# Optimization experiments

Measured on AMD Instinct MI355X. Metric: run time of the kernel, lower is better.

Reference implementation:

```python
import jax, jax.numpy as jnp
import numpy as np

B, L, C, H, W = 2, 4, 64, 80, 80
DISCRETE_RATIO, DOWNSAMPLE_RATE, NUM_ITER = 0.4, 2, 2


def _conv2d(x, w, b):
    y = jax.lax.conv_general_dilated(x, w, (1, 1), 'SAME',
                                     dimension_numbers=('NCHW', 'OIHW', 'NCHW'))
    return y + b[None, :, None, None]


def _get_transformation_matrix(M, h, w):
    # shift(center) @ [R 0; 0 1] @ shift(-center), then add raw translation (kornia-style)
    R = M[:, :2, :2]
    center = jnp.array([w / 2.0, h / 2.0], M.dtype)
    trans = center[None, :] - jnp.einsum('nij,j->ni', R, center) + M[:, :, 2]
    return jnp.concatenate([R, trans[:, :, None]], axis=2)  # (N,2,3)


def _warp_affine(src, M, mode):
    # src (N,C,h,w); M (N,2,3) maps src pixels -> dst pixels; sample src at M^{-1} @ dst
    # (equivalent to F.affine_grid/grid_sample with align_corners=True, zeros padding)
    N, Cc, h, w = src.shape
    bottom = jnp.tile(jnp.array([[[0.0, 0.0, 1.0]]], src.dtype), (N, 1, 1))
    Minv = jnp.linalg.inv(jnp.concatenate([M, bottom], axis=1))
    yy, xx = jnp.meshgrid(jnp.arange(h, dtype=src.dtype),
                          jnp.arange(w, dtype=src.dtype), indexing='ij')
    pts = jnp.stack([xx.ravel(), yy.ravel(), jnp.ones(h * w, src.dtype)], 0)  # (3,P)
    sp = jnp.einsum('nij,jp->nip', Minv, pts)
    sx, sy = sp[:, 0], sp[:, 1]  # (N,P) source pixel coords
    flat = src.reshape(N, Cc, h * w)

    def gather(ix, iy):
        valid = ((ix >= 0) & (ix < w) & (iy >= 0) & (iy < h)).astype(src.dtype)
        idx = jnp.clip(iy, 0, h - 1) * w + jnp.clip(ix, 0, w - 1)
        vals = jnp.take_along_axis(flat, jnp.broadcast_to(idx[:, None, :], (N, Cc, h * w)), axis=2)
        return vals * valid[:, None, :]

    if mode == 'nearest':
        out = gather(jnp.round(sx).astype(jnp.int32), jnp.round(sy).astype(jnp.int32))
    else:
        x0 = jnp.floor(sx); y0 = jnp.floor(sy)
        fx = (sx - x0)[:, None, :]; fy = (sy - y0)[:, None, :]
        x0 = x0.astype(jnp.int32); y0 = y0.astype(jnp.int32)
        out = (gather(x0, y0) * (1 - fx) * (1 - fy)
               + gather(x0 + 1, y0) * fx * (1 - fy)
               + gather(x0, y0 + 1) * (1 - fx) * fy
               + gather(x0 + 1, y0 + 1) * fx * fy)
    return out.reshape(N, Cc, h, w)


def _forward(x, pairwise_t_matrix, msg_w, msg_b, gates_w, gates_b, can_w, can_b, mlp_w, mlp_b):
    feats = x.reshape(B, L, C, H, W)
    # rows [0,1], cols [0,1,3] of the 4x4 SE(3) matrices; discretize translation
    t = pairwise_t_matrix[..., :2, :][..., jnp.array([0, 1, 3])]  # (B,L,L,2,3)
    t = t.at[..., 2].set(t[..., 2] / (DISCRETE_RATIO * DOWNSAMPLE_RATE))
    T = _get_transformation_matrix(t.reshape(-1, 2, 3), H, W)  # (B*L*L,2,3), flat index (b, j, i)
    mask = _warp_affine(jnp.ones((B * L * L, 1, H, W), x.dtype), T, 'nearest').reshape(B, L, L, 1, H, W)

    for _ in range(NUM_ITER):
        # 'b c h w -> b c w h' + flip(last): coordinate-convention fix (H==W)
        y = jnp.flip(jnp.swapaxes(feats, -1, -2), axis=-1)  # (B,L,C,H,W)
        # warp neighbor j into ego i frame with T[b,j,i]
        src = jnp.broadcast_to(y[:, :, None], (B, L, L, C, H, W)).reshape(-1, C, H, W)
        neighbor = _warp_affine(src, T, 'bilinear')
        ego = jnp.broadcast_to(y[:, None], (B, L, L, C, H, W)).reshape(-1, C, H, W)
        msg = _conv2d(jnp.concatenate([neighbor, ego], axis=1), msg_w, msg_b)
        msg = msg.reshape(B, L, L, C, H, W) * mask
        agg = msg.mean(axis=1)  # 'avg' over neighbors j -> (B,L,C,H,W)
        cat_feat = jnp.concatenate([y, agg], axis=2).reshape(B * L, 2 * C, H, W)
        # single ConvGRU step with zero initial hidden state
        h0 = jnp.zeros((B * L, C, H, W), x.dtype)
        gates = _conv2d(jnp.concatenate([cat_feat, h0], axis=1), gates_w, gates_b)
        reset = jax.nn.sigmoid(gates[:, :C])
        update = jax.nn.sigmoid(gates[:, C:])
        cand = jnp.tanh(_conv2d(jnp.concatenate([cat_feat, reset * h0], axis=1), can_w, can_b))
        h1 = (1.0 - update) * h0 + update * cand
        # undo the coordinate fix: flip(last) then 'c w h -> c h w'
        feats = jnp.swapaxes(jnp.flip(h1.reshape(B, L, C, H, W), axis=-1), -1, -2)

    out = feats[:, 0]  # ego agent of each sample, (B,C,H,W)
    return jnp.einsum('bchw,oc->bhwo', out, mlp_w) + mlp_b  # nn.Linear on channel-last


def setup_inputs() -> dict:
    key = jax.random.key(0)
    ks = jax.random.split(key, 12)
    x = jax.random.normal(ks[0], (B * L, C, H, W), dtype=jnp.float32)
    record_len = jnp.full((B,), L, dtype=jnp.int32)
    # realistic SE(2) pairwise transforms embedded in 4x4 homogeneous matrices
    ang = jax.random.uniform(ks[1], (B, L, L), minval=-0.3, maxval=0.3)
    tx = jax.random.uniform(ks[2], (B, L, L), minval=-8.0, maxval=8.0)
    ty = jax.random.uniform(ks[3], (B, L, L), minval=-8.0, maxval=8.0)
    c, s = jnp.cos(ang), jnp.sin(ang)
    z, o = jnp.zeros_like(ang), jnp.ones_like(ang)
    pairwise_t_matrix = jnp.stack([c, -s, z, tx,
                                   s, c, z, ty,
                                   z, z, o, z,
                                   z, z, z, o], axis=-1).reshape(B, L, L, 4, 4).astype(jnp.float32)
    prior_encoding = jax.random.normal(ks[4], (B * L, 3), dtype=jnp.float32)  # unused by forward
    sc = 0.05
    return {
        'x': x,
        'record_len': record_len,
        'pairwise_t_matrix': pairwise_t_matrix,
        'prior_encoding': prior_encoding,
        'msg_w': jax.random.normal(ks[5], (C, 2 * C, 3, 3), dtype=jnp.float32) * sc,
        'msg_b': jnp.zeros((C,), jnp.float32),
        'gates_w': jax.random.normal(ks[6], (2 * C, 3 * C, 3, 3), dtype=jnp.float32) * sc,
        'gates_b': jnp.zeros((2 * C,), jnp.float32),
        'can_w': jax.random.normal(ks[7], (C, 3 * C, 3, 3), dtype=jnp.float32) * sc,
        'can_b': jnp.zeros((C,), jnp.float32),
        'mlp_w': jax.random.normal(ks[8], (C, C), dtype=jnp.float32) * sc,
        'mlp_b': jnp.zeros((C,), jnp.float32),
    }


def reference(x, record_len, pairwise_t_matrix, prior_encoding,
              msg_w, msg_b, gates_w, gates_b, can_w, can_b, mlp_w, mlp_b):
    # record_len is fixed to L for every sample; prior_encoding is unused by the torch forward
    return _forward(x, pairwise_t_matrix, msg_w, msg_b, gates_w, gates_b,
                    can_w, can_b, mlp_w, mlp_b)
```

## Files before the change

kernel.cpp:

```cpp
#include <hip/hip_runtime.h>
#include <math.h>

#define WD 80
#define HW 6400
#define PW 82
#define PPX 6790
#define NIMG 8
#define NPAIR 32
#define TSTG 960

typedef short bf16x8 __attribute__((ext_vector_type(8)));
typedef float f32x4 __attribute__((ext_vector_type(4)));

__device__ __forceinline__ float bf2f(unsigned short u) {
    return __uint_as_float(((unsigned)u) << 16);
}
__device__ __forceinline__ unsigned short f2bf(float f) {
    unsigned u = __float_as_uint(f);
    u += 0x7fff + ((u >> 16) & 1);
    return (unsigned short)(u >> 16);
}

__device__ __forceinline__ void inv_affine(const float* __restrict__ P, int p, float* a) {
    const float* m = P + p * 16;
    float m00 = m[0], m01 = m[1], m02 = m[3] / 0.8f;
    float m10 = m[4], m11 = m[5], m12 = m[7] / 0.8f;
    float cx = 40.0f, cy = 40.0f;
    float tx = cx - (m00 * cx + m01 * cy) + m02;
    float ty = cy - (m10 * cx + m11 * cy) + m12;
    float id = 1.0f / (m00 * m11 - m01 * m10);
    a[0] =  m11 * id; a[1] = -m01 * id;
    a[3] = -m10 * id; a[4] =  m00 * id;
    a[2] = -(a[0] * tx + a[1] * ty);
    a[5] = -(a[3] * tx + a[4] * ty);
}

__global__ void prologue(const float* __restrict__ P, float* __restrict__ mats,
                         float* __restrict__ mask,
                         const float* __restrict__ msg_w, const float* __restrict__ gates_w,
                         const float* __restrict__ can_w,
                         unsigned short* __restrict__ Wn, unsigned short* __restrict__ We,
                         unsigned short* __restrict__ Wu, unsigned short* __restrict__ Wc) {
    int bx = blockIdx.x;
    if (bx < 32) {
        int p = bx;
        float a[6];
        inv_affine(P, p, a);
        if (threadIdx.x < 6) mats[p * 6 + threadIdx.x] = a[threadIdx.x];
        for (int q = threadIdx.x; q < HW; q += blockDim.x) {
            float x = (float)(q % WD), y = (float)(q / WD);
            float sx = a[0] * x + a[1] * y + a[2];
            float sy = a[3] * x + a[4] * y + a[5];
            int ix = (int)rintf(sx), iy = (int)rintf(sy);
            mask[p * HW + q] = (ix >= 0 && ix < WD && iy >= 0 && iy < WD) ? 1.0f : 0.0f;
        }
        return;
    }
    int t = (bx - 32) * 256 + threadIdx.x;
    if (t >= 221184) return;
    const float* src; unsigned short* dst;
    int cin_n, co_off, ci_off, stride, u;
    if (t < 36864)       { src = msg_w;   dst = Wn; cin_n = 64;  co_off = 0;  ci_off = 0;  stride = 1152; u = t; }
    else if (t < 73728)  { src = msg_w;   dst = We; cin_n = 64;  co_off = 0;  ci_off = 64; stride = 1152; u = t - 36864; }
    else if (t < 147456) { src = gates_w; dst = Wu; cin_n = 128; co_off = 64; ci_off = 0;  stride = 1728; u = t - 73728; }
    else                 { src = can_w;   dst = Wc; cin_n = 128; co_off = 0;  ci_off = 0;  stride = 1728; u = t - 147456; }
    int ci = u % cin_n;
    int co = (u / cin_n) & 63;
    int tap = u / (cin_n * 64);
    dst[u] = f2bf(src[(size_t)(co_off + co) * stride + (ci_off + ci) * 9 + tap]);
}

__global__ void zero_u4(uint4* __restrict__ p, int n4) {
    int t = blockIdx.x * blockDim.x + threadIdx.x;
    if (t < n4) p[t] = (uint4){0, 0, 0, 0};
}

__global__ __launch_bounds__(256) void rot_init_t(const float* __restrict__ x,
                                                  unsigned short* __restrict__ Y) {
    __shared__ float T[64][81];
    int img = blockIdx.x / 80, hh = blockIdx.x % 80;
    int tid = threadIdx.x;
    for (int idx = tid; idx < 64 * 80; idx += 256) {
        int c = idx / 80, ww = idx % 80;
        T[c][ww] = x[((size_t)(img * 64 + c) * 80 + hh) * 80 + ww];
    }
    __syncthreads();
    int b = 79 - hh;
    for (int idx = tid; idx < 80 * 64; idx += 256) {
        int a = idx >> 6, ch = idx & 63;
        Y[((size_t)img * PPX + (a + 1) * PW + (b + 1)) * 64 + ch] = f2bf(T[ch][a]);
    }
}

__global__ void warp_pairs(const unsigned short* __restrict__ Ysrc, const float* __restrict__ mats,
                           unsigned short* __restrict__ warped, int total, int only0) {
    int idx = blockIdx.x * blockDim.x + threadIdx.x;
    if (idx >= total) return;
    int g = idx & 7;
    int pp = (idx >> 3) % 6724;
    int k = idx / (6724 * 8);
    int p = only0 ? k * 4 : k;
    int py = pp / PW, pxx = pp % PW;
    uint4 v = {0, 0, 0, 0};
    if (py >= 1 && py <= 80 && pxx >= 1 && pxx <= 80) {
        int y = py - 1, x = pxx - 1;
        const float* a = mats + p * 6;
        float sx = a[0] * x + a[1] * y + a[2];
        float sy = a[3] * x + a[4] * y + a[5];
        float fxf = floorf(sx), fyf = floorf(sy);
        float fx = sx - fxf, fy = sy - fyf;
        int ix = (int)fxf, iy = (int)fyf;
        float w00 = (1.f - fx) * (1.f - fy), w10 = fx * (1.f - fy);
        float w01 = (1.f - fx) * fy,         w11 = fx * fy;
        bool vx0 = (unsigned)ix < WD, vx1 = (unsigned)(ix + 1) < WD;
        bool vy0 = (unsigned)iy < WD, vy1 = (unsigned)(iy + 1) < WD;
        if (!(vx0 && vy0)) w00 = 0.f;
        if (!(vx1 && vy0)) w10 = 0.f;
        if (!(vx0 && vy1)) w01 = 0.f;
        if (!(vx1 && vy1)) w11 = 0.f;
        int cx0 = min(max(ix, 0), WD - 1), cx1 = min(max(ix + 1, 0), WD - 1);
        int cy0 = min(max(iy, 0), WD - 1), cy1 = min(max(iy + 1, 0), WD - 1);
        const unsigned short* src = Ysrc + (size_t)(p >> 2) * PPX * 64 + g * 8;
        uint4 c00 = *(const uint4*)(src + ((cy0 + 1) * PW + cx0 + 1) * 64);
        uint4 c10 = *(const uint4*)(src + ((cy0 + 1) * PW + cx1 + 1) * 64);
        uint4 c01 = *(const uint4*)(src + ((cy1 + 1) * PW + cx0 + 1) * 64);
        uint4 c11 = *(const uint4*)(src + ((cy1 + 1) * PW + cx1 + 1) * 64);
        const unsigned short* p00 = (const unsigned short*)&c00;
        const unsigned short* p10 = (const unsigned short*)&c10;
        const unsigned short* p01 = (const unsigned short*)&c01;
        const unsigned short* p11 = (const unsigned short*)&c11;
        unsigned short r8[8];
#pragma unroll
        for (int kk = 0; kk < 8; ++kk) {
            float vv = w00 * bf2f(p00[kk]) + w10 * bf2f(p10[kk])
                     + w01 * bf2f(p01[kk]) + w11 * bf2f(p11[kk]);
            r8[kk] = f2bf(vv);
        }
        v = *(const uint4*)r8;
    }
    *(uint4*)(warped + ((size_t)k * PPX + pp) * 64 + g * 8) = v;
}

__device__ __forceinline__ void stage_t(const unsigned short* __restrict__ src,
                                        int x0, int y0, uint4* bufbase, int tid) {
    const int lane = tid & 63;
    const int wv = tid >> 6;
    for (int c = wv; c < TSTG / 64; c += 4) {
        int s = c * 64 + lane;
        int q = s >> 3;
        int yl = q / 20, xl = q - yl * 20;
        int g = (s & 7) ^ (q & 7);
        const unsigned short* gp = src + ((y0 + yl) * PW + x0 + xl) * 64 + g * 8;
        __builtin_amdgcn_global_load_lds(
            (const __attribute__((address_space(1))) unsigned int*)gp,
            (__attribute__((address_space(3))) unsigned int*)(bufbase + c * 64),
            16, 0, 0);
    }
}

__device__ __forceinline__ void load_w(const unsigned short* __restrict__ W, int row,
                                       int cinstride, int cin0, int lh, bf16x8* Wf) {
#pragma unroll
    for (int ks = 0; ks < 2; ++ks)
#pragma unroll
        for (int tap = 0; tap < 9; ++tap)
            Wf[ks * 9 + tap] = *(const bf16x8*)(W + (size_t)(tap * 64 + row) * cinstride
                                                + cin0 + ks * 32 + lh * 8);
}

__device__ __forceinline__ void conv_pass4(const uint4* __restrict__ buf, const bf16x8* Wf,
                                           int ll, int lh, f32x4* acc) {
#pragma unroll
    for (int ks = 0; ks < 2; ++ks) {
        const int g = ks * 4 + lh;
#pragma unroll
        for (int tx = 0; tx < 3; ++tx) {
            bf16x8 A[6];
#pragma unroll
            for (int s = 0; s < 6; ++s) {
                int q = s * 20 + tx + ll;
                A[s] = *(const bf16x8*)&buf[q * 8 + (g ^ (q & 7))];
            }
#pragma unroll
            for (int ty = 0; ty < 3; ++ty) {
                bf16x8 B = Wf[ks * 9 + ty * 3 + tx];
#pragma unroll
                for (int r = 0; r < 4; ++r)
                    acc[r] = __builtin_amdgcn_mfma_f32_16x16x32_bf16(A[r + ty], B, acc[r], 0, 0, 0);
            }
        }
    }
}

__global__ __launch_bounds__(256, 2) void msg_agg(const unsigned short* __restrict__ warped,
        const unsigned short* __restrict__ Y, const float* __restrict__ mask,
        const unsigned short* __restrict__ Wn, const unsigned short* __restrict__ We,
        const float* __restrict__ bias, unsigned short* __restrict__ Gpad, int only0) {
    __shared__ uint4 lds[2 * TSTG];
    __shared__ float lmask[4][4][16];
    const int tid = threadIdx.x, lane = tid & 63, wv = tid >> 6;
    const int ll = lane & 15, lh = lane >> 4;
    const int x0 = blockIdx.x * 16, y0 = blockIdx.y * 4;
    const int t = blockIdx.z;
    const int b = only0 ? t : (t >> 2), j = only0 ? 0 : (t & 3);
    const int img = only0 ? t * 4 : t;
    const int row = wv * 16 + ll;

    int ks_[4];
#pragma unroll
    for (int i = 0; i < 4; ++i)
        ks_[i] = only0 ? (b * 4 + i) : ((b * 4 + i) * 4 + j);
    {
        int i = tid >> 6, r = (tid >> 4) & 3, px = tid & 15;
        int p = only0 ? ks_[i] * 4 : ks_[i];
        lmask[i][r][px] = mask[(size_t)p * HW + (y0 + r) * WD + x0 + px];
    }
    bf16x8 Wf[18];
    load_w(Wn, row, 64, 0, lh, Wf);
    stage_t(warped + (size_t)ks_[0] * PPX * 64, x0, y0, lds, tid);
    __syncthreads();

    f32x4 tot[4];
    float msum[4][4];
#pragma unroll
    for (int r = 0; r < 4; ++r) {
        tot[r] = (f32x4){0.f, 0.f, 0.f, 0.f};
#pragma unroll
        for (int jj = 0; jj < 4; ++jj) msum[r][jj] = 0.f;
    }

    for (int i = 0; i < 4; ++i) {
        if (i < 3)
            stage_t(warped + (size_t)ks_[i + 1] * PPX * 64, x0, y0, lds + ((i + 1) & 1) * TSTG, tid);
        else
            stage_t(Y + (size_t)img * PPX * 64, x0, y0, lds, tid);
        f32x4 acc[4];
#pragma unroll
        for (int r = 0; r < 4; ++r) acc[r] = (f32x4){0.f, 0.f, 0.f, 0.f};
        conv_pass4(lds + (i & 1) * TSTG, Wf, ll, lh, acc);
#pragma unroll
        for (int r = 0; r < 4; ++r)
#pragma unroll
            for (int jj = 0; jj < 4; ++jj) {
                float m = lmask[i][r][lh * 4 + jj];
                msum[r][jj] += m;
                tot[r][jj] += m * acc[r][jj];
            }
        __syncthreads();
    }

    load_w(We, row, 64, 0, lh, Wf);
    f32x4 acc[4];
#pragma unroll
    for (int r = 0; r < 4; ++r) acc[r] = (f32x4){0.f, 0.f, 0.f, 0.f};
    conv_pass4(lds, Wf, ll, lh, acc);

    float bv = bias[row];
#pragma unroll
    for (int r = 0; r < 4; ++r)
#pragma unroll
        for (int jj = 0; jj < 4; ++jj) {
            int x = x0 + lh * 4 + jj;
            float val = 0.25f * (tot[r][jj] + msum[r][jj] * (acc[r][jj] + bv));
            Gpad[((size_t)t * PPX + (y0 + r + 1) * PW + (x + 1)) * 64 + row] = f2bf(val);
        }
}

__global__ __launch_bounds__(256, 2) void gru_conv(const unsigned short* __restrict__ Ysrc,
        const unsigned short* __restrict__ Gpad,
        const unsigned short* __restrict__ Wu, const unsigned short* __restrict__ Wc,
        const float* __restrict__ bu, const float* __restrict__ bc,
        unsigned short* __restrict__ Ydst, int only0) {
    __shared__ uint4 lds[2 * TSTG];
    const int tid = threadIdx.x, lane = tid & 63, wv = tid >> 6;
    const int ll = lane & 15, lh = lane >> 4;
    const int x0 = blockIdx.x * 16, y0 = blockIdx.y * 4;
    const int t = blockIdx.z;
    const int img = only0 ? t * 4 : t;
    const int row = wv * 16 + ll;

    stage_t(Ysrc + (size_t)img * PPX * 64, x0, y0, lds, tid);
    stage_t(Gpad + (size_t)t * PPX * 64, x0, y0, lds + TSTG, tid);
    bf16x8 W0[18], W1[18];
    load_w(Wu, row, 128, 0,  lh, W0);
    load_w(Wu, row, 128, 64, lh, W1);
    __syncthreads();

    f32x4 aU[4], aC[4];
#pragma unroll
    for (int r = 0; r < 4; ++r) {
        aU[r] = (f32x4){0.f, 0.f, 0.f, 0.f};
        aC[r] = (f32x4){0.f, 0.f, 0.f, 0.f};
    }
    conv_pass4(lds,        W0, ll, lh, aU);
    load_w(Wc, row, 128, 0,  lh, W0);
    conv_pass4(lds + TSTG, W1, ll, lh, aU);
    load_w(Wc, row, 128, 64, lh, W1);
    conv_pass4(lds,        W0, ll, lh, aC);
    conv_pass4(lds + TSTG, W1, ll, lh, aC);

    float ub = bu[row], cb = bc[row];
#pragma unroll
    for (int r = 0; r < 4; ++r)
#pragma unroll
        for (int jj = 0; jj < 4; ++jj) {
            int x = x0 + lh * 4 + jj;
            float u = 1.f / (1.f + __expf(-(aU[r][jj] + ub)));
            float e2 = __expf(2.f * (aC[r][jj] + cb));
            float c = (e2 - 1.f) / (e2 + 1.f);
            Ydst[((size_t)img * PPX + (y0 + r + 1) * PW + (x + 1)) * 64 + row] = f2bf(u * c);
        }
}

__global__ void final_mlp(const unsigned short* __restrict__ yfin, const float* __restrict__ mw,
                          const float* __restrict__ mb, float* __restrict__ out) {
    int t = blockIdx.x * blockDim.x + threadIdx.x;
    if (t >= 2 * HW * 64) return;
    int o  = t & 63;
    int wv = (t >> 6) % WD;
    int h  = ((t >> 6) / WD) % WD;
    int b  = t / (HW * 64);
    const unsigned short* src = yfin + ((size_t)(b * 4) * PPX + (wv + 1) * PW + (80 - h)) * 64;
    const float* wrow = mw + o * 64;
    float r = mb[o];
#pragma unroll
    for (int c8 = 0; c8 < 8; ++c8) {
        bf16x8 v = *(const bf16x8*)(src + c8 * 8);
#pragma unroll
        for (int k = 0; k < 8; ++k)
            r += bf2f(((const unsigned short*)&v)[k]) * wrow[c8 * 8 + k];
    }
    out[t] = r;
}

extern "C" void kernel_launch(void* const* d_in, const int* in_sizes, int n_in,
                              void* d_out, int out_size, void* d_ws, size_t ws_size,
                              hipStream_t stream) {
    const float* x       = (const float*)d_in[0];
    const float* P       = (const float*)d_in[2];
    const float* msg_w   = (const float*)d_in[4];
    const float* msg_b   = (const float*)d_in[5];
    const float* gates_w = (const float*)d_in[6];
    const float* gates_b = (const float*)d_in[7];
    const float* can_w   = (const float*)d_in[8];
    const float* can_b   = (const float*)d_in[9];
    const float* mlp_w   = (const float*)d_in[10];
    const float* mlp_b   = (const float*)d_in[11];
    float* out = (float*)d_out;

    char* wsb = (char*)d_ws;
    float* mats = (float*)wsb;
    float* mask = (float*)(wsb + 1024);
    unsigned short* Wn = (unsigned short*)(wsb + 820224);
    unsigned short* We = Wn + 36864;
    unsigned short* Wu = We + 36864;
    unsigned short* Wc = Wu + 73728;
    unsigned short* Y0 = Wc + 73728;
    unsigned short* Y1 = Y0 + (size_t)NIMG * PPX * 64;
    unsigned short* Gpad = Y1 + (size_t)NIMG * PPX * 64;
    unsigned short* warped = Gpad + (size_t)NIMG * PPX * 64;

    {
        int n4 = (int)((size_t)3 * NIMG * PPX * 64 * 2 / 16);
        zero_u4<<<(n4 + 255) / 256, 256, 0, stream>>>((uint4*)Y0, n4);
    }
    prologue<<<32 + (221184 + 255) / 256, 256, 0, stream>>>(P, mats, mask,
        msg_w, gates_w, can_w, Wn, We, Wu, Wc);
    rot_init_t<<<NIMG * 80, 256, 0, stream>>>(x, Y0);

    warp_pairs<<<(32 * 6724 * 8 + 255) / 256, 256, 0, stream>>>(Y0, mats, warped, 32 * 6724 * 8, 0);
    msg_agg<<<dim3(5, 20, 8), 256, 0, stream>>>(warped, Y0, mask, Wn, We, msg_b, Gpad, 0);
    gru_conv<<<dim3(5, 20, 8), 256, 0, stream>>>(Y0, Gpad, Wu, Wc, gates_b + 64, can_b, Y1, 0);

    warp_pairs<<<(8 * 6724 * 8 + 255) / 256, 256, 0, stream>>>(Y1, mats, warped, 8 * 6724 * 8, 1);
    msg_agg<<<dim3(5, 20, 2), 256, 0, stream>>>(warped, Y1, mask, Wn, We, msg_b, Gpad, 1);
    gru_conv<<<dim3(5, 20, 2), 256, 0, stream>>>(Y1, Gpad, Wu, Wc, gates_b + 64, can_b, Y0, 1);

    final_mlp<<<(2 * HW * 64 + 255) / 256, 256, 0, stream>>>(Y0, mlp_w, mlp_b, out);
}
```

Measured before the change: 247.3 us.

## Zero only padded borders, cut register use in msg_agg and gru_conv

Rather than zeroing all three padded activation buffers in full, only the one-pixel border ring of each padded image is cleared, since every interior pixel is overwritten later. In msg_agg the running per-pixel mask sum is dropped and recomputed from the LDS mask at the end. gru_conv keeps a single weight fragment array and reloads it before each pass instead of holding two. These changes lower register pressure so more waves can be resident, at the cost of serialising weight loads with the MFMA passes.

```diff
diff --git a/kernel.cpp b/kernel.cpp
--- a/kernel.cpp
+++ b/kernel.cpp
@@ -70,9 +70,18 @@
     dst[u] = f2bf(src[(size_t)(co_off + co) * stride + (ci_off + ci) * 9 + tap]);
 }
 
-__global__ void zero_u4(uint4* __restrict__ p, int n4) {
-    int t = blockIdx.x * blockDim.x + threadIdx.x;
-    if (t < n4) p[t] = (uint4){0, 0, 0, 0};
+__global__ void zero_borders(unsigned short* __restrict__ bufs) {
+    int idx = blockIdx.x * blockDim.x + threadIdx.x;
+    if (idx >= 24 * 324 * 8) return;
+    int g = idx & 7;
+    int e = (idx >> 3) % 324;
+    int img = idx / (324 * 8);
+    int pp;
+    if (e < 82)       pp = e;
+    else if (e < 164) pp = 81 * PW + (e - 82);
+    else if (e < 244) pp = (e - 164 + 1) * PW;
+    else              pp = (e - 244 + 1) * PW + 81;
+    *(uint4*)(bufs + ((size_t)img * PPX + pp) * 64 + g * 8) = (uint4){0, 0, 0, 0};
 }
 
 __global__ __launch_bounds__(256) void rot_init_t(const float* __restrict__ x,
@@ -221,13 +230,8 @@
     __syncthreads();
 
     f32x4 tot[4];
-    float msum[4][4];
-#pragma unroll
-    for (int r = 0; r < 4; ++r) {
-        tot[r] = (f32x4){0.f, 0.f, 0.f, 0.f};
-#pragma unroll
-        for (int jj = 0; jj < 4; ++jj) msum[r][jj] = 0.f;
-    }
+#pragma unroll
+    for (int r = 0; r < 4; ++r) tot[r] = (f32x4){0.f, 0.f, 0.f, 0.f};
 
     for (int i = 0; i < 4; ++i) {
         if (i < 3)
@@ -241,11 +245,8 @@
 #pragma unroll
         for (int r = 0; r < 4; ++r)
 #pragma unroll
-            for (int jj = 0; jj < 4; ++jj) {
-                float m = lmask[i][r][lh * 4 + jj];
-                msum[r][jj] += m;
-                tot[r][jj] += m * acc[r][jj];
-            }
+            for (int jj = 0; jj < 4; ++jj)
+                tot[r][jj] += lmask[i][r][lh * 4 + jj] * acc[r][jj];
         __syncthreads();
     }
 
@@ -260,9 +261,10 @@
     for (int r = 0; r < 4; ++r)
 #pragma unroll
         for (int jj = 0; jj < 4; ++jj) {
-            int x = x0 + lh * 4 + jj;
-            float val = 0.25f * (tot[r][jj] + msum[r][jj] * (acc[r][jj] + bv));
-            Gpad[((size_t)t * PPX + (y0 + r + 1) * PW + (x + 1)) * 64 + row] = f2bf(val);
+            int px = lh * 4 + jj;
+            float msum = lmask[0][r][px] + lmask[1][r][px] + lmask[2][r][px] + lmask[3][r][px];
+            float val = 0.25f * (tot[r][jj] + msum * (acc[r][jj] + bv));
+            Gpad[((size_t)t * PPX + (y0 + r + 1) * PW + (x0 + px + 1)) * 64 + row] = f2bf(val);
         }
 }
 
@@ -281,9 +283,8 @@
 
     stage_t(Ysrc + (size_t)img * PPX * 64, x0, y0, lds, tid);
     stage_t(Gpad + (size_t)t * PPX * 64, x0, y0, lds + TSTG, tid);
-    bf16x8 W0[18], W1[18];
-    load_w(Wu, row, 128, 0,  lh, W0);
-    load_w(Wu, row, 128, 64, lh, W1);
+    bf16x8 Wf[18];
+    load_w(Wu, row, 128, 0, lh, Wf);
     __syncthreads();
 
     f32x4 aU[4], aC[4];
@@ -292,12 +293,13 @@
         aU[r] = (f32x4){0.f, 0.f, 0.f, 0.f};
         aC[r] = (f32x4){0.f, 0.f, 0.f, 0.f};
     }
-    conv_pass4(lds,        W0, ll, lh, aU);
-    load_w(Wc, row, 128, 0,  lh, W0);
-    conv_pass4(lds + TSTG, W1, ll, lh, aU);
-    load_w(Wc, row, 128, 64, lh, W1);
-    conv_pass4(lds,        W0, ll, lh, aC);
-    conv_pass4(lds + TSTG, W1, ll, lh, aC);
+    conv_pass4(lds, Wf, ll, lh, aU);
+    load_w(Wu, row, 128, 64, lh, Wf);
+    conv_pass4(lds + TSTG, Wf, ll, lh, aU);
+    load_w(Wc, row, 128, 0, lh, Wf);
+    conv_pass4(lds, Wf, ll, lh, aC);
+    load_w(Wc, row, 128, 64, lh, Wf);
+    conv_pass4(lds + TSTG, Wf, ll, lh, aC);
 
     float ub = bu[row], cb = bc[row];
 #pragma unroll
@@ -360,10 +362,7 @@
     unsigned short* Gpad = Y1 + (size_t)NIMG * PPX * 64;
     unsigned short* warped = Gpad + (size_t)NIMG * PPX * 64;
 
-    {
-        int n4 = (int)((size_t)3 * NIMG * PPX * 64 * 2 / 16);
-        zero_u4<<<(n4 + 255) / 256, 256, 0, stream>>>((uint4*)Y0, n4);
-    }
+    zero_borders<<<(24 * 324 * 8 + 255) / 256, 256, 0, stream>>>(Y0);
     prologue<<<32 + (221184 + 255) / 256, 256, 0, stream>>>(P, mats, mask,
         msg_w, gates_w, can_w, Wn, We, Wu, Wc);
     rot_init_t<<<NIMG * 80, 256, 0, stream>>>(x, Y0);
```

Result: faster. 237.9 us (-3.8%).
